# Kernel optimization log

Hardware: AMD Instinct MI355X
Metric: run time of the kernel (lower is better)

Reference implementation:

```python
import jax, jax.numpy as jnp
import numpy as np

GRID_DIMS = (64, 64, 64)
GRID_LOWER = np.array([0.0, 0.0, 0.0], np.float32)
GRID_STEPS = np.array([0.015625, 0.015625, 0.015625], np.float32)
RADIUS = 0.03125
STENCIL = 2  # ceil(radius / step)


def _poly6(d2, h):
    # standard SPH poly6 smoothing kernel: 315/(64 pi h^9) (h^2 - d^2)^3, d <= h
    c = np.float32(315.0 / (64.0 * np.pi * h ** 9))
    return jnp.where(d2 <= h * h, c * (h * h - d2) ** 3, 0.0)


def particles2grid(locs, data, density):
    # locs [B,N,3], data [B,N,C], density [B,N] -> grid [B,X,Y,Z,C]
    B, N, _ = locs.shape
    C = data.shape[-1]
    X, Y, Z = GRID_DIMS
    dims = jnp.array(GRID_DIMS, jnp.int32)
    r = jnp.arange(-STENCIL, STENCIL + 1)
    offs = jnp.stack(jnp.meshgrid(r, r, r, indexing='ij'), -1).reshape(-1, 3)  # [K,3]
    base = jnp.floor((locs - GRID_LOWER) / GRID_STEPS).astype(jnp.int32)        # [B,N,3]
    cells = base[:, :, None, :] + offs                                          # [B,N,K,3]
    centers = GRID_LOWER + (cells.astype(locs.dtype) + 0.5) * GRID_STEPS
    d2 = jnp.sum((centers - locs[:, :, None, :]) ** 2, -1)                      # [B,N,K]
    w = _poly6(d2, RADIUS)
    w = jnp.where(jnp.all((cells >= 0) & (cells < dims), -1), w, 0.0)
    contrib = w[..., None] * (data / density[..., None])[:, :, None, :]         # [B,N,K,C]
    cells = jnp.clip(cells, 0, dims - 1)
    flat = (cells[..., 0] * Y + cells[..., 1]) * Z + cells[..., 2]              # [B,N,K]

    def splat(f, c):
        return jnp.zeros((X * Y * Z, C), data.dtype).at[f.reshape(-1)].add(c.reshape(-1, C))

    return jax.vmap(splat)(flat, contrib).reshape(B, X, Y, Z, C)


def grid2particles(grid, locs):
    # trilinear interpolation of grid [B,X,Y,Z,C] at particle locations [B,N,3]
    B, X, Y, Z, C = grid.shape
    dims = jnp.array([X, Y, Z], jnp.int32)
    pos = (locs - GRID_LOWER) / GRID_STEPS - 0.5                                # cell-center coords
    i0 = jnp.floor(pos).astype(jnp.int32)
    frac = pos - i0.astype(locs.dtype)
    gflat = grid.reshape(B, X * Y * Z, C)
    gather = jax.vmap(lambda g, f: g[f])                                        # [B,N] -> [B,N,C]
    out = jnp.zeros((B, locs.shape[1], C), grid.dtype)
    for dx in (0, 1):
        for dy in (0, 1):
            for dz in (0, 1):
                off = jnp.array([dx, dy, dz], jnp.int32)
                idx = i0 + off
                wd = jnp.where(off == 1, frac, 1.0 - frac)                      # [B,N,3]
                w = wd[..., 0] * wd[..., 1] * wd[..., 2]
                w = jnp.where(jnp.all((idx >= 0) & (idx < dims), -1), w, 0.0)
                idx = jnp.clip(idx, 0, dims - 1)
                flat = (idx[..., 0] * Y + idx[..., 1]) * Z + idx[..., 2]
                out = out + w[..., None] * gather(gflat, flat)
    return out


def conv3d(x, w, b):
    y = jax.lax.conv_general_dilated(x, w, (1, 1, 1), 'SAME',
                                     dimension_numbers=('NCDHW', 'OIDHW', 'NCDHW'))
    return y + b[None, :, None, None, None]


def prelu(x, a):
    return jnp.where(x >= 0, x, a * x)


def setup_inputs() -> dict:
    key = jax.random.key(0)
    ks = jax.random.split(key, 8)
    B, N = 2, 32768
    Cin, K, Cout = 4, 32, 4
    s = lambda fan: np.float32(1.0 / np.sqrt(fan * 27))
    return {
        'locs': jax.random.uniform(ks[0], (B, N, 3), jnp.float32),
        'data': jax.random.normal(ks[1], (B, N, Cin), jnp.float32),
        'density': jax.random.uniform(ks[2], (B, N), jnp.float32, 0.5, 1.5),
        'W0': jax.random.normal(ks[3], (K, Cin, 3, 3, 3), jnp.float32) * s(Cin),
        'b0': jnp.zeros((K,), jnp.float32),
        'W1': jax.random.normal(ks[4], (K, K, 3, 3, 3), jnp.float32) * s(K),
        'b1': jnp.zeros((K,), jnp.float32),
        'W2': jax.random.normal(ks[5], (K, K, 3, 3, 3), jnp.float32) * s(K),
        'b2': jnp.zeros((K,), jnp.float32),
        'W3': jax.random.normal(ks[6], (Cout, K, 3, 3, 3), jnp.float32) * s(K),
        'b3': jnp.zeros((Cout,), jnp.float32),
        'a0': jnp.full((1,), 0.25, jnp.float32),
        'a1': jnp.full((1,), 0.25, jnp.float32),
        'a2': jnp.full((1,), 0.25, jnp.float32),
    }


def reference(locs, data, density, W0, b0, W1, b1, W2, b2, W3, b3, a0, a1, a2):
    grid = particles2grid(locs, data, density)            # [B,X,Y,Z,Cin]
    g = jnp.transpose(grid, (0, 4, 1, 2, 3))              # NCDHW
    g = prelu(conv3d(g, W0, b0), a0)
    g = prelu(conv3d(g, W1, b1), a1)
    g = prelu(conv3d(g, W2, b2), a2)
    g = conv3d(g, W3, b3)
    g = jnp.transpose(g, (0, 2, 3, 4, 1))                 # [B,X,Y,Z,Cout]
    return grid2particles(g, locs)                        # [B,N,Cout]
```

## Files before the change

kernel.cpp:

```cpp
#include <hip/hip_runtime.h>

#define BATCH 2
#define NPART 32768
#define GD 64
#define NVOX (BATCH * GD * GD * GD)

typedef unsigned short ushortT;
typedef __attribute__((ext_vector_type(8))) short short8;
typedef __attribute__((ext_vector_type(16))) float float16;

__device__ __forceinline__ float poly6_c() {
    const double H9 = 1.0 / 35184372088832.0;
    return (float)(315.0 / (64.0 * 3.14159265358979323846 * H9));
}

__device__ __forceinline__ ushortT bf16_rne(float f) {
    unsigned int u = __float_as_uint(f);
    u = (u + 0x7fffu + ((u >> 16) & 1u)) >> 16;
    return (ushortT)u;
}

__device__ __forceinline__ int imax(int a, int b) { return a > b ? a : b; }
__device__ __forceinline__ int imin(int a, int b) { return a < b ? a : b; }

__device__ __forceinline__ void load_lds16(const void* g, void* l) {
    __builtin_amdgcn_global_load_lds(
        (const __attribute__((address_space(1))) void*)g,
        (__attribute__((address_space(3))) void*)l, 16, 0, 0);
}

__global__ __launch_bounds__(256) void prep_kernel(
    int* __restrict__ zp,
    const float* __restrict__ W0, const float* __restrict__ W1,
    const float* __restrict__ W2, const float* __restrict__ W3,
    short* __restrict__ Bp) {
    int bid = blockIdx.x, tid = threadIdx.x;
    if (bid < 513) {
        int t = bid * 256 + tid;
        if (t < 131088) zp[t] = 0;
        return;
    }
    int t = (bid - 513) * 256 + tid;
    if (t >= 176 * 512) return;
    int kt = t >> 9;
    int l = (t >> 3) & 63, j = t & 7;
    int n = l & 31, q = l >> 5;
    float v = 0.f;
    if (kt < 14) {
        int k = kt * 16 + 8 * q + j;
        int tap = k >> 3, ic = k & 7;
        if (tap < 27 && ic < 4) v = W0[(n * 4 + ic) * 27 + tap];
    } else {
        const float* W; int O, s;
        if (kt < 68)       { W = W1; O = 32; s = kt - 14; }
        else if (kt < 122) { W = W2; O = 32; s = kt - 68; }
        else               { W = W3; O = 4;  s = kt - 122; }
        int h = s / 27, ss = s - h * 27;
        int gI = ss / 3, dy = ss - gI * 3;
        int dx = gI / 3, dz = gI - dx * 3;
        int tap = dx * 9 + dy * 3 + dz;
        int ic = h * 16 + q * 8 + j;
        if (n < O) v = W[(n * 32 + ic) * 27 + tap];
    }
    Bp[t] = (short)bf16_rne(v);
}

__global__ __launch_bounds__(256) void bin_count_kernel(
    const float* __restrict__ locs, int* __restrict__ counts) {
    int t = blockIdx.x * blockDim.x + threadIdx.x;
    if (t >= BATCH * NPART) return;
    int b = t >> 15;
    int bx = ((int)floorf(locs[t * 3 + 0] * 64.0f)) >> 1;
    int by = ((int)floorf(locs[t * 3 + 1] * 64.0f)) >> 1;
    int bz = ((int)floorf(locs[t * 3 + 2] * 64.0f)) >> 1;
    atomicAdd(&counts[b * 32768 + ((bx * 32) + by) * 32 + bz], 1);
}

__global__ __launch_bounds__(256) void scanA_kernel(
    const int* __restrict__ counts, int* __restrict__ offsets,
    int* __restrict__ blockSum) {
    __shared__ int sh[256];
    int tid = threadIdx.x, g = blockIdx.x;
    int v = counts[g * 256 + tid];
    sh[tid] = v;
    __syncthreads();
    for (int off = 1; off < 256; off <<= 1) {
        int u = (tid >= off) ? sh[tid - off] : 0;
        __syncthreads();
        sh[tid] += u;
        __syncthreads();
    }
    offsets[g * 256 + tid] = sh[tid] - v;
    if (tid == 255) blockSum[g] = sh[255];
}

__global__ __launch_bounds__(256) void scanB_kernel(
    int* __restrict__ offsets, const int* __restrict__ blockSum) {
    __shared__ int sh[256];
    int tid = threadIdx.x, g = blockIdx.x;
    sh[tid] = (tid < g) ? blockSum[tid] : 0;
    __syncthreads();
    for (int off = 128; off > 0; off >>= 1) {
        if (tid < off) sh[tid] += sh[tid + off];
        __syncthreads();
    }
    offsets[g * 256 + tid] += sh[0];
    if (g == 255 && tid == 255) offsets[65536] = BATCH * NPART;
}

__global__ __launch_bounds__(256) void bin_scatter_kernel(
    const float* __restrict__ locs, const float* __restrict__ data,
    const float* __restrict__ density, const int* __restrict__ offsets,
    int* __restrict__ cursor, float* __restrict__ payload) {
    int t = blockIdx.x * blockDim.x + threadIdx.x;
    if (t >= BATCH * NPART) return;
    int b = t >> 15;
    float px = locs[t * 3 + 0];
    float py = locs[t * 3 + 1];
    float pz = locs[t * 3 + 2];
    int bx = ((int)floorf(px * 64.0f)) >> 1;
    int by = ((int)floorf(py * 64.0f)) >> 1;
    int bz = ((int)floorf(pz * 64.0f)) >> 1;
    int bb = b * 32768 + ((bx * 32) + by) * 32 + bz;
    int slot = atomicAdd(&cursor[bb], 1);
    int idx = offsets[bb] + slot;
    float inv_d = 1.0f / density[t];
    float4 p0 = {px, py, pz, data[t * 4 + 0] * inv_d};
    float4 p1 = {data[t * 4 + 1] * inv_d, data[t * 4 + 2] * inv_d,
                 data[t * 4 + 3] * inv_d, 0.f};
    *(float4*)(payload + idx * 8)     = p0;
    *(float4*)(payload + idx * 8 + 4) = p1;
}

__global__ __launch_bounds__(256) void splat_gather_kernel(
    const float* __restrict__ payload, const int* __restrict__ offsets,
    ushortT* __restrict__ g8) {
    __shared__ float plist[256 * 8];
    __shared__ int segS[36];
    __shared__ int segP[37];
    __shared__ int shTot[1];

    int wg = blockIdx.x;
    int sb = wg & 511, b = wg >> 9;
    int X0 = (sb >> 6) * 8, Y0 = ((sb >> 3) & 7) * 8, Z0 = (sb & 7) * 8;
    int tid = threadIdx.x;

    int bxlo = imax(0, (X0 - 2) >> 1), bxhi = imin(31, (X0 + 9) >> 1);
    int bylo = imax(0, (Y0 - 2) >> 1), byhi = imin(31, (Y0 + 9) >> 1);
    int bzlo = imax(0, (Z0 - 2) >> 1), bzhi = imin(31, (Z0 + 9) >> 1);
    int ny = byhi - bylo + 1;
    int ns = (bxhi - bxlo + 1) * ny;
    if (tid < ns) {
        int bx = bxlo + tid / ny, by = bylo + tid % ny;
        int row = b * 32768 + (bx * 32 + by) * 32;
        int s = offsets[row + bzlo];
        int e = offsets[row + bzhi + 1];
        segS[tid] = s;
        segP[tid] = e - s;
    }
    __syncthreads();
    if (tid == 0) {
        int p = 0;
        for (int k = 0; k < ns; ++k) { int len = segP[k]; segP[k] = p; p += len; }
        segP[ns] = p;
        shTot[0] = p;
    }
    __syncthreads();

    const float step = 0.015625f;
    const float h2 = 0.03125f * 0.03125f;
    const float cc = poly6_c();
    int total = shTot[0];

    int l = tid & 63, w = tid >> 6;
    int cx = X0 + 4 * (w >> 1) + (l >> 4);
    int cy = Y0 + 4 * (w & 1) + ((l >> 2) & 3);
    int cz0 = Z0 + (l & 3);
    float xc  = ((float)cx  + 0.5f) * step;
    float yc  = ((float)cy  + 0.5f) * step;
    float zc0 = ((float)cz0 + 0.5f) * step;
    float zc1 = zc0 + 4.0f * step;

    float a00 = 0.f, a01 = 0.f, a02 = 0.f, a03 = 0.f;
    float a10 = 0.f, a11 = 0.f, a12 = 0.f, a13 = 0.f;

    int nchunks = (total + 255) >> 8;
    for (int ch = 0; ch < nchunks; ++ch) {
        __syncthreads();
        int jj = (ch << 8) + tid;
        if (jj < total) {
            int k = 0;
            while (jj >= segP[k + 1]) ++k;
            int idx = segS[k] + (jj - segP[k]);
            *(float4*)(plist + tid * 8)     = *(const float4*)(payload + idx * 8);
            *(float4*)(plist + tid * 8 + 4) = *(const float4*)(payload + idx * 8 + 4);
        }
        __syncthreads();
        int cnt = imin(256, total - (ch << 8));
        for (int p = 0; p < cnt; ++p) {
            float4 pa = *(const float4*)(plist + p * 8);
            float dx = pa.x - xc, dy = pa.y - yc;
            float dxy2 = fmaf(dy, dy, dx * dx);
            if (!__any(dxy2 <= h2)) continue;
            float4 pv = *(const float4*)(plist + p * 8 + 4);
            float dz0 = pa.z - zc0;
            float d20 = fmaf(dz0, dz0, dxy2);
            float u0 = fmaxf(h2 - d20, 0.f);
            float w0 = (cc * u0) * (u0 * u0);
            a00 = fmaf(w0, pa.w, a00);
            a01 = fmaf(w0, pv.x, a01);
            a02 = fmaf(w0, pv.y, a02);
            a03 = fmaf(w0, pv.z, a03);
            float dz1 = pa.z - zc1;
            float d21 = fmaf(dz1, dz1, dxy2);
            float u1 = fmaxf(h2 - d21, 0.f);
            float w1 = (cc * u1) * (u1 * u1);
            a10 = fmaf(w1, pa.w, a10);
            a11 = fmaf(w1, pv.x, a11);
            a12 = fmaf(w1, pv.y, a12);
            a13 = fmaf(w1, pv.z, a13);
        }
    }

    size_t cellBase = (size_t)(((b * 64 + cx) * 64 + cy) * 64);
    short8 o;
    o[0] = (short)bf16_rne(a00); o[1] = (short)bf16_rne(a01);
    o[2] = (short)bf16_rne(a02); o[3] = (short)bf16_rne(a03);
    o[4] = 0; o[5] = 0; o[6] = 0; o[7] = 0;
    *(short8*)(g8 + (cellBase + cz0) * 8) = o;
    o[0] = (short)bf16_rne(a10); o[1] = (short)bf16_rne(a11);
    o[2] = (short)bf16_rne(a12); o[3] = (short)bf16_rne(a13);
    *(short8*)(g8 + (cellBase + cz0 + 4) * 8) = o;
}

template <int ICG, int KT, bool FINAL>
__global__ __launch_bounds__(256, 2) void mfma_conv_kernel(
    const ushortT* __restrict__ in, const short* __restrict__ Bpack,
    const float* __restrict__ bias, const float* __restrict__ alpha,
    const float* __restrict__ zguard, void* __restrict__ outv) {
    constexpr int CIN  = ICG * 8;
    constexpr int PH   = (ICG == 1) ? 1 : 2;
    constexpr int NCHP = (ICG == 1) ? (36 * 34) : (36 * 2 * 34);
    constexpr int BUFS = NCHP * 8;
    __shared__ short lds[2 * BUFS];

    int wg2 = ((blockIdx.x & 7) << 6) | (blockIdx.x >> 3);
    int yq = wg2 & 15, xp = (wg2 >> 4) & 15, b = wg2 >> 8;
    int X0 = xp * 4, Y0 = yq * 4;
    int tid = threadIdx.x;
    const ushortT* inb = in + (size_t)b * (64 * 64 * 64 * CIN);

    int l = tid & 63, w = tid >> 6;
    int n = l & 31, q = l >> 5;
    int laneZ = (l & 31) * 8;
    const short* bp = Bpack + (size_t)l * 8;
    float bval = FINAL ? (n < 4 ? bias[n] : 0.f) : bias[n];

    auto stage = [&](int ph) {
        int t = ph / PH, h = ph - t * PH;
        int zb = t * 32;
        short* dst = lds + (ph & 1) * BUFS;
#pragma unroll
        for (int it = 0; it < (NCHP + 255) / 256; ++it) {
            int ccid = it * 256 + tid;
            if (ccid < NCHP) {
                int col, icg2, zi;
                if constexpr (ICG == 1) {
                    col = ccid / 34; zi = ccid - col * 34; icg2 = 0;
                } else {
                    col = ccid / 68;
                    int rem = ccid - col * 68;
                    icg2 = rem / 34; zi = rem - icg2 * 34;
                }
                int gx = X0 + col / 6 - 1;
                int gy = Y0 + col % 6 - 1;
                int gz = zb + zi - 1;
                const void* src = (const void*)zguard;
                if ((unsigned)gx < 64u && (unsigned)gy < 64u && (unsigned)gz < 64u)
                    src = (const void*)(inb +
                        ((size_t)(((gx * 64) + gy) * 64 + gz)) * CIN + (h * 2 + icg2) * 8);
                load_lds16(src, (void*)(dst + ccid * 8));
            }
        }
    };

    stage(0);

#pragma unroll
    for (int tile = 0; tile < 2; ++tile) {
        int Z0 = tile * 32;
        float16 acc0, acc1, acc2, acc3;
#pragma unroll
        for (int r = 0; r < 16; ++r) {
            acc0[r] = bval; acc1[r] = bval; acc2[r] = bval; acc3[r] = bval;
        }

#pragma unroll
        for (int h = 0; h < PH; ++h) {
            int ph = tile * PH + h;
            __syncthreads();
            if (ph + 1 < 2 * PH) stage(ph + 1);
            const short* lb = lds + (ph & 1) * BUFS;

            if constexpr (ICG == 1) {
                short8 bf[4];
#pragma unroll
                for (int i = 0; i < 4; ++i) bf[i] = *(const short8*)(bp + i * 512);
#pragma unroll
                for (int kt = 0; kt < KT; ++kt) {
                    short8 bcur = bf[kt & 3];
                    if (kt + 4 < KT) bf[kt & 3] = *(const short8*)(bp + (kt + 4) * 512);
                    int tap0 = kt * 2, tap1 = kt * 2 + 1;
                    if (tap1 > 26) tap1 = 26;
                    int dx0 = tap0 / 9, r0 = tap0 - dx0 * 9, dy0 = r0 / 3, dz0 = r0 - dy0 * 3;
                    int dx1 = tap1 / 9, r1 = tap1 - dx1 * 9, dy1 = r1 / 3, dz1 = r1 - dy1 * 3;
#define AOFS1(c) (q ? ((((w + dx1) * 6 + ((c) + dy1)) * 34 + dz1) * 8) \
                    : ((((w + dx0) * 6 + ((c) + dy0)) * 34 + dz0) * 8))
                    short8 a0 = *(const short8*)(lb + AOFS1(0) + laneZ);
                    short8 a1 = *(const short8*)(lb + AOFS1(1) + laneZ);
                    short8 a2 = *(const short8*)(lb + AOFS1(2) + laneZ);
                    short8 a3 = *(const short8*)(lb + AOFS1(3) + laneZ);
#undef AOFS1
                    __builtin_amdgcn_s_setprio(1);
                    acc0 = __builtin_amdgcn_mfma_f32_32x32x16_bf16(a0, bcur, acc0, 0, 0, 0);
                    acc1 = __builtin_amdgcn_mfma_f32_32x32x16_bf16(a1, bcur, acc1, 0, 0, 0);
                    acc2 = __builtin_amdgcn_mfma_f32_32x32x16_bf16(a2, bcur, acc2, 0, 0, 0);
                    acc3 = __builtin_amdgcn_mfma_f32_32x32x16_bf16(a3, bcur, acc3, 0, 0, 0);
                    __builtin_amdgcn_s_setprio(0);
                }
            } else {
                short8 bf[4];
#pragma unroll
                for (int i = 0; i < 4; ++i)
                    bf[i] = *(const short8*)(bp + (h * 27 + i) * 512);
#pragma unroll
                for (int g = 0; g < 9; ++g) {
                    int dx = g / 3, dz = g - dx * 3;
                    short8 fr[6];
#pragma unroll
                    for (int col = 0; col < 6; ++col) {
                        int ofs = ((((w + dx) * 6 + col) * 2 + q) * 34 + dz) * 8;
                        fr[col] = *(const short8*)(lb + ofs + laneZ);
                    }
#pragma unroll
                    for (int dy = 0; dy < 3; ++dy) {
                        int k27 = g * 3 + dy;
                        short8 bcur = bf[k27 & 3];
                        if (k27 + 4 < 27)
                            bf[k27 & 3] = *(const short8*)(bp + (h * 27 + k27 + 4) * 512);
                        __builtin_amdgcn_s_setprio(1);
                        acc0 = __builtin_amdgcn_mfma_f32_32x32x16_bf16(fr[0 + dy], bcur, acc0, 0, 0, 0);
                        acc1 = __builtin_amdgcn_mfma_f32_32x32x16_bf16(fr[1 + dy], bcur, acc1, 0, 0, 0);
                        acc2 = __builtin_amdgcn_mfma_f32_32x32x16_bf16(fr[2 + dy], bcur, acc2, 0, 0, 0);
                        acc3 = __builtin_amdgcn_mfma_f32_32x32x16_bf16(fr[3 + dy], bcur, acc3, 0, 0, 0);
                        __builtin_amdgcn_s_setprio(0);
                    }
                }
            }
        }

        size_t base0 = (size_t)(((b * 64 + X0 + w) * 64 + Y0) * 64) + Z0;
        if constexpr (FINAL) {
            float* out = (float*)outv;
            if (n < 4) {
#pragma unroll
                for (int r = 0; r < 16; ++r) {
                    int z = (r & 3) + 8 * (r >> 2) + 4 * q;
                    out[(base0 + z) * 4 + n]        = acc0[r];
                    out[(base0 + 64 + z) * 4 + n]   = acc1[r];
                    out[(base0 + 128 + z) * 4 + n]  = acc2[r];
                    out[(base0 + 192 + z) * 4 + n]  = acc3[r];
                }
            }
        } else {
            float a = alpha[0];
            ushortT* out = (ushortT*)outv;
#pragma unroll
            for (int r = 0; r < 16; ++r) {
                int z = (r & 3) + 8 * (r >> 2) + 4 * q;
                float v0 = acc0[r]; v0 = v0 >= 0.f ? v0 : a * v0;
                out[(base0 + z) * 32 + n] = bf16_rne(v0);
                float v1 = acc1[r]; v1 = v1 >= 0.f ? v1 : a * v1;
                out[(base0 + 64 + z) * 32 + n] = bf16_rne(v1);
                float v2 = acc2[r]; v2 = v2 >= 0.f ? v2 : a * v2;
                out[(base0 + 128 + z) * 32 + n] = bf16_rne(v2);
                float v3 = acc3[r]; v3 = v3 >= 0.f ? v3 : a * v3;
                out[(base0 + 192 + z) * 32 + n] = bf16_rne(v3);
            }
        }
    }
}

__global__ __launch_bounds__(256) void gather_kernel(
    const float* __restrict__ grid, const float* __restrict__ locs,
    float* __restrict__ out) {
    int t = blockIdx.x * blockDim.x + threadIdx.x;
    if (t >= BATCH * NPART) return;
    int b = t >> 15;

    float px = locs[t * 3 + 0] * 64.0f - 0.5f;
    float py = locs[t * 3 + 1] * 64.0f - 0.5f;
    float pz = locs[t * 3 + 2] * 64.0f - 0.5f;
    int ix = (int)floorf(px);
    int iy = (int)floorf(py);
    int iz = (int)floorf(pz);
    float fx = px - (float)ix;
    float fy = py - (float)iy;
    float fz = pz - (float)iz;

    const float* gb = grid + (size_t)b * GD * GD * GD * 4;
    float o0 = 0.f, o1 = 0.f, o2 = 0.f, o3 = 0.f;

#pragma unroll
    for (int dx = 0; dx < 2; ++dx) {
        int x = ix + dx;
        if ((unsigned)x > 63u) continue;
        float wx = dx ? fx : 1.0f - fx;
#pragma unroll
        for (int dy = 0; dy < 2; ++dy) {
            int y = iy + dy;
            if ((unsigned)y > 63u) continue;
            float wy = dy ? fy : 1.0f - fy;
#pragma unroll
            for (int dz = 0; dz < 2; ++dz) {
                int z = iz + dz;
                if ((unsigned)z > 63u) continue;
                float wz = dz ? fz : 1.0f - fz;
                float w = wx * wy * wz;
                const float4 g = *(const float4*)(gb + (size_t)(((x * GD) + y) * GD + z) * 4);
                o0 += w * g.x; o1 += w * g.y; o2 += w * g.z; o3 += w * g.w;
            }
        }
    }
    out[t * 4 + 0] = o0;
    out[t * 4 + 1] = o1;
    out[t * 4 + 2] = o2;
    out[t * 4 + 3] = o3;
}

extern "C" void kernel_launch(void* const* d_in, const int* in_sizes, int n_in,
                              void* d_out, int out_size, void* d_ws, size_t ws_size,
                              hipStream_t stream) {
    const float* locs    = (const float*)d_in[0];
    const float* data    = (const float*)d_in[1];
    const float* density = (const float*)d_in[2];
    const float* W0 = (const float*)d_in[3];
    const float* b0 = (const float*)d_in[4];
    const float* W1 = (const float*)d_in[5];
    const float* b1 = (const float*)d_in[6];
    const float* W2 = (const float*)d_in[7];
    const float* b2 = (const float*)d_in[8];
    const float* W3 = (const float*)d_in[9];
    const float* b3 = (const float*)d_in[10];
    const float* a0 = (const float*)d_in[11];
    const float* a1 = (const float*)d_in[12];
    const float* a2 = (const float*)d_in[13];
    float* out = (float*)d_out;

    char* ws = (char*)d_ws;
    ushortT* g8  = (ushortT*)(ws);
    ushortT* gA  = (ushortT*)(ws + 8388608);
    ushortT* gB  = (ushortT*)(ws + 41943040);
    float*  gF   = (float*)(ws + 75497472);
    short*  Bp   = (short*)(ws + 83886080);
    short*  Bp0  = Bp;
    short*  Bp1  = Bp + 14 * 512;
    short*  Bp2  = Bp + 68 * 512;
    short*  Bp3  = Bp + 122 * 512;
    float* zguard   = (float*)(ws + 84066240);
    int*   counts   = (int*)(ws + 84066304);
    int*   cursor   = (int*)(ws + 84328448);
    int*   offsets  = (int*)(ws + 84590592);
    int*   blockSum = (int*)(ws + 84852752);
    float* payload  = (float*)(ws + 84853888);

    prep_kernel<<<513 + 352, 256, 0, stream>>>((int*)zguard, W0, W1, W2, W3, Bp);

    bin_count_kernel<<<(BATCH * NPART) / 256, 256, 0, stream>>>(locs, counts);
    scanA_kernel<<<256, 256, 0, stream>>>(counts, offsets, blockSum);
    scanB_kernel<<<256, 256, 0, stream>>>(offsets, blockSum);
    bin_scatter_kernel<<<(BATCH * NPART) / 256, 256, 0, stream>>>(
        locs, data, density, offsets, cursor, payload);

    splat_gather_kernel<<<BATCH * 512, 256, 0, stream>>>(payload, offsets, g8);

    const int CGRID = 512;
    mfma_conv_kernel< 1, 14, false><<<CGRID, 256, 0, stream>>>(g8, Bp0, b0, a0, zguard, gA);
    mfma_conv_kernel< 4, 54, false><<<CGRID, 256, 0, stream>>>(gA, Bp1, b1, a1, zguard, gB);
    mfma_conv_kernel< 4, 54, false><<<CGRID, 256, 0, stream>>>(gB, Bp2, b2, a2, zguard, gA);
    mfma_conv_kernel< 4, 54, true ><<<CGRID, 256, 0, stream>>>(gA, Bp3, b3, b3, zguard, gF);

    gather_kernel<<<(BATCH * NPART) / 256, 256, 0, stream>>>(gF, locs, out);
}
```

Baseline: 242.9 us.

## Halve conv block tile in X and remap waves to a 2x2 layout

```diff
diff --git a/kernel.cpp b/kernel.cpp
--- a/kernel.cpp
+++ b/kernel.cpp
@@ -234,23 +234,24 @@
 }
 
 template <int ICG, int KT, bool FINAL>
-__global__ __launch_bounds__(256, 2) void mfma_conv_kernel(
+__global__ __launch_bounds__(256, 3) void mfma_conv_kernel(
     const ushortT* __restrict__ in, const short* __restrict__ Bpack,
     const float* __restrict__ bias, const float* __restrict__ alpha,
     const float* __restrict__ zguard, void* __restrict__ outv) {
     constexpr int CIN  = ICG * 8;
     constexpr int PH   = (ICG == 1) ? 1 : 2;
-    constexpr int NCHP = (ICG == 1) ? (36 * 34) : (36 * 2 * 34);
+    constexpr int NCHP = (ICG == 1) ? (24 * 34) : (24 * 2 * 34);
     constexpr int BUFS = NCHP * 8;
     __shared__ short lds[2 * BUFS];
 
-    int wg2 = ((blockIdx.x & 7) << 6) | (blockIdx.x >> 3);
-    int yq = wg2 & 15, xp = (wg2 >> 4) & 15, b = wg2 >> 8;
-    int X0 = xp * 4, Y0 = yq * 4;
+    int wg = ((blockIdx.x & 7) << 7) | (blockIdx.x >> 3);
+    int yq = wg & 15, xp = (wg >> 4) & 31, b = wg >> 9;
+    int X0 = xp * 2, Y0 = yq * 4;
     int tid = threadIdx.x;
     const ushortT* inb = in + (size_t)b * (64 * 64 * 64 * CIN);
 
     int l = tid & 63, w = tid >> 6;
+    int wx = w >> 1, wy2 = (w & 1) * 2;
     int n = l & 31, q = l >> 5;
     int laneZ = (l & 31) * 8;
     const short* bp = Bpack + (size_t)l * 8;
@@ -289,11 +290,9 @@
 #pragma unroll
     for (int tile = 0; tile < 2; ++tile) {
         int Z0 = tile * 32;
-        float16 acc0, acc1, acc2, acc3;
-#pragma unroll
-        for (int r = 0; r < 16; ++r) {
-            acc0[r] = bval; acc1[r] = bval; acc2[r] = bval; acc3[r] = bval;
-        }
+        float16 acc0, acc1;
+#pragma unroll
+        for (int r = 0; r < 16; ++r) { acc0[r] = bval; acc1[r] = bval; }
 
 #pragma unroll
         for (int h = 0; h < PH; ++h) {
@@ -314,18 +313,14 @@
                     if (tap1 > 26) tap1 = 26;
                     int dx0 = tap0 / 9, r0 = tap0 - dx0 * 9, dy0 = r0 / 3, dz0 = r0 - dy0 * 3;
                     int dx1 = tap1 / 9, r1 = tap1 - dx1 * 9, dy1 = r1 / 3, dz1 = r1 - dy1 * 3;
-#define AOFS1(c) (q ? ((((w + dx1) * 6 + ((c) + dy1)) * 34 + dz1) * 8) \
-                    : ((((w + dx0) * 6 + ((c) + dy0)) * 34 + dz0) * 8))
-                    short8 a0 = *(const short8*)(lb + AOFS1(0) + laneZ);
-                    short8 a1 = *(const short8*)(lb + AOFS1(1) + laneZ);
-                    short8 a2 = *(const short8*)(lb + AOFS1(2) + laneZ);
-                    short8 a3 = *(const short8*)(lb + AOFS1(3) + laneZ);
+#define AOFS1(c) (q ? ((((wx + dx1) * 6 + ((c) + dy1)) * 34 + dz1) * 8) \
+                    : ((((wx + dx0) * 6 + ((c) + dy0)) * 34 + dz0) * 8))
+                    short8 a0 = *(const short8*)(lb + AOFS1(wy2) + laneZ);
+                    short8 a1 = *(const short8*)(lb + AOFS1(wy2 + 1) + laneZ);
 #undef AOFS1
                     __builtin_amdgcn_s_setprio(1);
                     acc0 = __builtin_amdgcn_mfma_f32_32x32x16_bf16(a0, bcur, acc0, 0, 0, 0);
                     acc1 = __builtin_amdgcn_mfma_f32_32x32x16_bf16(a1, bcur, acc1, 0, 0, 0);
-                    acc2 = __builtin_amdgcn_mfma_f32_32x32x16_bf16(a2, bcur, acc2, 0, 0, 0);
-                    acc3 = __builtin_amdgcn_mfma_f32_32x32x16_bf16(a3, bcur, acc3, 0, 0, 0);
                     __builtin_amdgcn_s_setprio(0);
                 }
             } else {
@@ -336,11 +331,11 @@
 #pragma unroll
                 for (int g = 0; g < 9; ++g) {
                     int dx = g / 3, dz = g - dx * 3;
-                    short8 fr[6];
-#pragma unroll
-                    for (int col = 0; col < 6; ++col) {
-                        int ofs = ((((w + dx) * 6 + col) * 2 + q) * 34 + dz) * 8;
-                        fr[col] = *(const short8*)(lb + ofs + laneZ);
+                    short8 fr[4];
+#pragma unroll
+                    for (int k = 0; k < 4; ++k) {
+                        int ofs = ((((wx + dx) * 6 + (wy2 + k)) * 2 + q) * 34 + dz) * 8;
+                        fr[k] = *(const short8*)(lb + ofs + laneZ);
                     }
 #pragma unroll
                     for (int dy = 0; dy < 3; ++dy) {
@@ -351,25 +346,21 @@
                         __builtin_amdgcn_s_setprio(1);
                         acc0 = __builtin_amdgcn_mfma_f32_32x32x16_bf16(fr[0 + dy], bcur, acc0, 0, 0, 0);
                         acc1 = __builtin_amdgcn_mfma_f32_32x32x16_bf16(fr[1 + dy], bcur, acc1, 0, 0, 0);
-                        acc2 = __builtin_amdgcn_mfma_f32_32x32x16_bf16(fr[2 + dy], bcur, acc2, 0, 0, 0);
-                        acc3 = __builtin_amdgcn_mfma_f32_32x32x16_bf16(fr[3 + dy], bcur, acc3, 0, 0, 0);
                         __builtin_amdgcn_s_setprio(0);
                     }
                 }
             }
         }
 
-        size_t base0 = (size_t)(((b * 64 + X0 + w) * 64 + Y0) * 64) + Z0;
+        size_t base0 = (size_t)(((b * 64 + X0 + wx) * 64 + (Y0 + wy2)) * 64) + Z0;
         if constexpr (FINAL) {
             float* out = (float*)outv;
             if (n < 4) {
 #pragma unroll
                 for (int r = 0; r < 16; ++r) {
                     int z = (r & 3) + 8 * (r >> 2) + 4 * q;
-                    out[(base0 + z) * 4 + n]        = acc0[r];
-                    out[(base0 + 64 + z) * 4 + n]   = acc1[r];
-                    out[(base0 + 128 + z) * 4 + n]  = acc2[r];
-                    out[(base0 + 192 + z) * 4 + n]  = acc3[r];
+                    out[(base0 + z) * 4 + n]      = acc0[r];
+                    out[(base0 + 64 + z) * 4 + n] = acc1[r];
                 }
             }
         } else {
@@ -382,10 +373,6 @@
                 out[(base0 + z) * 32 + n] = bf16_rne(v0);
                 float v1 = acc1[r]; v1 = v1 >= 0.f ? v1 : a * v1;
                 out[(base0 + 64 + z) * 32 + n] = bf16_rne(v1);
-                float v2 = acc2[r]; v2 = v2 >= 0.f ? v2 : a * v2;
-                out[(base0 + 128 + z) * 32 + n] = bf16_rne(v2);
-                float v3 = acc3[r]; v3 = v3 >= 0.f ? v3 : a * v3;
-                out[(base0 + 192 + z) * 32 + n] = bf16_rne(v3);
             }
         }
     }
@@ -484,7 +471,7 @@
 
     splat_gather_kernel<<<BATCH * 512, 256, 0, stream>>>(payload, offsets, g8);
 
-    const int CGRID = 512;
+    const int CGRID = 1024;
     mfma_conv_kernel< 1, 14, false><<<CGRID, 256, 0, stream>>>(g8, Bp0, b0, a0, zguard, gA);
     mfma_conv_kernel< 4, 54, false><<<CGRID, 256, 0, stream>>>(gA, Bp1, b1, a1, zguard, gB);
     mfma_conv_kernel< 4, 54, false><<<CGRID, 256, 0, stream>>>(gB, Bp2, b2, a2, zguard, gA);
```

After: 277.9 us. 14.4% more time.
